# Optimization experiments

Hardware: AMD Instinct MI355X
Metric: run time of the kernel (lower is better)

Reference implementation:

```python
import jax, jax.numpy as jnp
import numpy as np

# Frankenstein DNC dims (from __init__ defaults, L reduced 16->8 for memory budget)
X = 47764; H = 128; L = 8; VT = 3620; W = 32; R = 8; N = 512; BS = 1
D = X + R * W + 2 * H            # RNN_Unit input width = 48276
ET = W * R + 3 * W + 5 * R + 3   # interface width = 395
EPS = 1e-8


def setup_inputs() -> dict:
    key = jax.random.key(0)
    ks = jax.random.split(key, 16)
    su = 1.0 / np.sqrt(H)          # nn.Linear default-style scale
    sv = 1.0 / np.sqrt(VT)
    se = 1.0 / np.sqrt(ET)
    u = lambda k, shp, s: jax.random.uniform(k, shp, jnp.float32, -s, s)
    return {
        'x_in': jax.random.normal(ks[0], (BS, X), jnp.float32),
        # stacked per-layer LSTM-gate weights (L, D, H) / biases (L, H)
        'W_i': u(ks[1], (L, D, H), su), 'b_i': u(ks[2], (L, H), su),
        'W_f': u(ks[3], (L, D, H), su), 'b_f': u(ks[4], (L, H), su),
        'W_o': u(ks[5], (L, D, H), su), 'b_o': u(ks[6], (L, H), su),
        'W_s': u(ks[7], (L, D, H), su), 'b_s': u(ks[8], (L, H), su),
        'W_y': u(ks[9], (L * H, VT), sv),
        'W_E': u(ks[10], (L * H, ET), se),
        'W_r': u(ks[11], (W * R, VT), sv),
        # memory / state buffers (requires_grad=False in torch)
        'memory': jax.random.uniform(ks[12], (N, W), jnp.float32, -1.0, 1.0),
        'last_read_vector': jnp.zeros((BS, W, R), jnp.float32),
        'hidden_prev': jnp.zeros((BS, L, H), jnp.float32),
        'old_states': jnp.zeros((L, BS, H), jnp.float32),
        'precedence': jnp.zeros((BS, N), jnp.float32),
        'linkage': jnp.zeros((BS, N, N), jnp.float32),
        'last_read_weightings': jnp.zeros((BS, N, R), jnp.float32),
        'last_usage': jnp.zeros((BS, N), jnp.float32),
        'last_write_weighting': jnp.zeros((BS, N), jnp.float32),
    }


def reference(x_in, W_i, b_i, W_f, b_f, W_o, b_o, W_s, b_s, W_y, W_E, W_r,
              memory, last_read_vector, hidden_prev, old_states, precedence,
              linkage, last_read_weightings, last_usage, last_write_weighting):
    # ---- controller: L stacked LSTM-like units, sequential over layers ----
    input_x_t = jnp.concatenate([x_in, last_read_vector.reshape(BS, -1)], axis=1)
    hpt = jnp.transpose(hidden_prev, (1, 0, 2))  # (L, BS, H)

    def layer(h_prev_layer, xs):
        Wi, bi, Wf, bf, Wo, bo, Ws, bs_, hp, os_ = xs
        si = jnp.concatenate([input_x_t, hp, h_prev_layer], axis=1)  # (BS, D)
        ig = jax.nn.sigmoid(si @ Wi + bi)
        fg = jax.nn.sigmoid(si @ Wf + bf)
        st = fg * os_ + ig * jnp.tanh(si @ Ws + bs_)
        og = jax.nn.sigmoid(si @ Wo + bo)
        h = og * jnp.tanh(st)
        return h, h

    _, hs = jax.lax.scan(layer, jnp.zeros((BS, H), x_in.dtype),
                         (W_i, b_i, W_f, b_f, W_o, b_o, W_s, b_s, hpt, old_states))
    flat = jnp.transpose(hs, (1, 0, 2)).reshape(BS, L * H)
    output = flat @ W_y
    E = flat @ W_E

    # ---- interface vector parsing ----
    i0 = 0
    read_keys = E[:, :W * R].reshape(BS, W, R); i0 = W * R
    read_strengths = 1.0 - jax.nn.log_sigmoid(E[:, i0:i0 + R]); i0 += R
    write_key = E[:, i0:i0 + W]; i0 += W
    write_strength = 1.0 - jax.nn.log_sigmoid(E[:, i0:i0 + 1]); i0 += 1
    erase = jax.nn.sigmoid(E[:, i0:i0 + W]); i0 += W
    write_vec = E[:, i0:i0 + W]; i0 += W
    free_gates = jax.nn.sigmoid(E[:, i0:i0 + R]); i0 += R
    alloc_gate = jax.nn.sigmoid(E[:, i0:i0 + 1]); i0 += 1
    write_gate = jax.nn.sigmoid(E[:, i0:i0 + 1]); i0 += 1
    read_modes = jax.nn.softmax(E[:, i0:i0 + 3 * R].reshape(BS, R, 3), axis=2)

    # ---- memory retention, usage, allocation ----
    psi = jnp.prod(1.0 - free_gates[:, None, :] * last_read_weightings, axis=2)  # (BS,N)
    usage = (last_usage + last_write_weighting - last_usage * last_write_weighting) * psi
    idx = jnp.argsort(usage, axis=1)
    su = jnp.take_along_axis(usage, idx, axis=1)
    cp = jnp.cumprod(su, axis=1)
    excl = jnp.concatenate([jnp.ones((BS, 1), usage.dtype), cp[:, :-1]], axis=1)
    alloc = jnp.take_along_axis((1.0 - su) * excl, jnp.argsort(idx, axis=1), axis=1)

    # ---- write weighting (content + allocation) ----
    Mn = memory / jnp.maximum(jnp.linalg.norm(memory, axis=1, keepdims=True), EPS)
    kn = write_key / jnp.maximum(jnp.linalg.norm(write_key, axis=1, keepdims=True), EPS)
    cw = jax.nn.softmax(write_strength * (kn @ Mn.T), axis=1)  # (BS,N)
    ww = write_gate * (alloc_gate * alloc + (1.0 - alloc_gate) * cw)

    # ---- write to memory (bs == 1) ----
    memory_new = memory * (1.0 - jnp.einsum('bn,bw->nw', ww, erase)) \
                 + jnp.einsum('bn,bw->nw', ww, write_vec)

    # ---- temporal linkage ----
    Lm = (1.0 - ww[:, :, None] - ww[:, None, :]) * linkage \
         + ww[:, :, None] * precedence[:, None, :]
    Lm = Lm * (1.0 - jnp.eye(N, dtype=Lm.dtype))[None]
    fw = jnp.einsum('bij,bjr->bir', Lm, last_read_weightings)   # forward weighting
    bw = jnp.einsum('bji,bjr->bir', Lm, last_read_weightings)   # backward weighting

    # ---- read weightings and read vectors ----
    Mn2 = memory_new / jnp.maximum(jnp.linalg.norm(memory_new, axis=1, keepdims=True), EPS)
    knr = read_keys / jnp.maximum(jnp.linalg.norm(read_keys, axis=1, keepdims=True), EPS)
    cr = jax.nn.softmax(read_strengths[:, None, :] * jnp.einsum('nw,bwr->bnr', Mn2, knr), axis=1)
    rw = bw * read_modes[:, None, :, 0] + cr * read_modes[:, None, :, 1] \
         + fw * read_modes[:, None, :, 2]                        # (BS,N,R)
    rv = jnp.einsum('nw,bnr->bwr', memory_new, rw)               # (BS,W,R)

    y = output + rv.reshape(BS, W * R) @ W_r                     # (BS, v_t)
    return y
```

## Files before the change

### kernel.cpp

```cpp
#include <hip/hip_runtime.h>
#include <math.h>

#define XDIM 47764
#define HDIM 128
#define LDIM 8
#define VTDIM 3620
#define WDIM 32
#define RDIM 8
#define NDIM 512
#define RW 256
#define DDIM 48276
#define FIXED 48148
#define ETDIM 395
#define EPSV 1e-8f

#define CHUNK 768
#define NCHUNK 63
#define K1_COMPUTE (32 * NCHUNK)
#define K1_COPYB 128

#define OFF_FIXED   258048
#define OFF_WREC    262144
#define OFF_FLAT    786432
#define OFF_ERAW    787456
#define OFF_WW      787968
#define OFF_MEMNEW  788480
#define OFF_CR      804864
#define OFF_RM      808960
#define OFF_FW      808992
#define OFF_BW      813088
#define OFF_RV      817184

typedef float f4 __attribute__((ext_vector_type(4)));

__device__ __forceinline__ f4 ntload4(const float* p) {
    return __builtin_nontemporal_load((const f4*)p);
}

__device__ inline float sigm(float x) { return 1.f / (1.f + expf(-x)); }
__device__ inline float log_sigmoid(float x) {
    return (x >= 0.f) ? -log1pf(expf(-x)) : (x - log1pf(expf(x)));
}

__global__ __launch_bounds__(256) void k1_partial(
    const float* __restrict__ x_in, const float* __restrict__ lrv,
    const float* __restrict__ hprev,
    const float* __restrict__ Wi, const float* __restrict__ Wf,
    const float* __restrict__ Wo, const float* __restrict__ Ws,
    float* __restrict__ ws, float* __restrict__ out)
{
    const int bid = blockIdx.x;
    const int t   = threadIdx.x;

    if (bid >= K1_COMPUTE) {
        int cb = bid - K1_COMPUTE;
        #pragma unroll
        for (int r = 0; r < 4; ++r) {
            int idx4  = cb * 1024 + r * 256 + t;
            int flat  = idx4 << 2;
            int combo = flat >> 14;
            int rem   = flat & 16383;
            int j = rem >> 7, h = rem & 127;
            int g = combo >> 3, l = combo & 7;
            const float* Wg = (g == 0) ? Wi : (g == 1) ? Wf : (g == 2) ? Wo : Ws;
            float4 v = *reinterpret_cast<const float4*>(
                Wg + ((size_t)l * DDIM + FIXED + j) * HDIM + h);
            *reinterpret_cast<float4*>(ws + OFF_WREC + flat) = v;
        }
        if (cb == 0) { ws[OFF_ERAW + t] = 0.f; ws[OFF_ERAW + 256 + t] = 0.f; }
        else if (cb == 1) {
            #pragma unroll
            for (int r = 0; r < 8; ++r) out[r * 256 + t] = 0.f;
        } else if (cb == 2) {
            #pragma unroll
            for (int r = 0; r < 7; ++r) {
                int v = 2048 + r * 256 + t;
                if (v < VTDIM) out[v] = 0.f;
            }
        }
        return;
    }

    const int combo = bid / NCHUNK;
    const int chunk = bid % NCHUNK;
    const int g = combo >> 3, l = combo & 7;
    const float* __restrict__ Wg = (g == 0) ? Wi : (g == 1) ? Wf : (g == 2) ? Wo : Ws;
    const int d0 = chunk * CHUNK;

    __shared__ float s_lds[CHUNK];
    for (int i = t; i < CHUNK; i += 256) {
        int d = d0 + i;
        float v = 0.f;
        if (d < XDIM)            v = x_in[d];
        else if (d < XDIM + RW)  v = lrv[d - XDIM];
        else if (d < FIXED)      v = hprev[l * HDIM + (d - XDIM - RW)];
        s_lds[i] = v;
    }
    __syncthreads();

    const int c4 = t & 15;
    const int p  = t >> 4;
    const int r0 = p * 48;
    const float* wp = Wg + ((size_t)l * DDIM + d0 + r0) * HDIM + (c4 << 2);

    f4 a = {0.f, 0.f, 0.f, 0.f};
    f4 b = {0.f, 0.f, 0.f, 0.f};

    if (chunk != NCHUNK - 1) {
        #pragma unroll 4
        for (int i = 0; i < 48; ++i) {
            float s = s_lds[r0 + i];
            const f4 w0 = ntload4(wp);
            const f4 w1 = ntload4(wp + 64);
            wp += HDIM;
            a += s * w0;
            b += s * w1;
        }
    } else {
        for (int i = 0; i < 48; ++i) {
            if (d0 + r0 + i >= FIXED) break;
            float s = s_lds[r0 + i];
            const f4 w0 = ntload4(wp);
            const f4 w1 = ntload4(wp + 64);
            wp += HDIM;
            a += s * w0;
            b += s * w1;
        }
    }

    __shared__ f4 red[16][32];
    red[p][c4]      = a;
    red[p][c4 + 16] = b;
    __syncthreads();
    if (t < 32) {
        f4 s = red[0][t];
        #pragma unroll
        for (int q = 1; q < 16; ++q) s += red[q][t];
        float* fx = ws + OFF_FIXED + combo * HDIM + (t << 2);
        atomicAdd(fx + 0, s.x);
        atomicAdd(fx + 1, s.y);
        atomicAdd(fx + 2, s.z);
        atomicAdd(fx + 3, s.w);
    }
}

__global__ __launch_bounds__(1024) void k3_recurrent(
    const float* __restrict__ bi, const float* __restrict__ bf,
    const float* __restrict__ bo, const float* __restrict__ bs,
    const float* __restrict__ old_states, float* __restrict__ ws)
{
    const int t = threadIdx.x;
    const int g = t >> 8;
    const int q = (t >> 7) & 1;
    const int h = t & 127;

    __shared__ float hp[128];
    __shared__ float gl[4][2][128];

    float fx[8];
    const float* bg = (g == 0) ? bi : (g == 1) ? bf : (g == 2) ? bo : bs;
    if (q == 0) {
        #pragma unroll
        for (int l = 0; l < LDIM; ++l)
            fx[l] = ws[OFF_FIXED + (g * 8 + l) * HDIM + h] + bg[l * HDIM + h];
    }
    if (t < 128) hp[t] = 0.f;
    __syncthreads();

    for (int l = 0; l < LDIM; ++l) {
        int combo = g * 8 + l;
        float acc = (q == 0) ? fx[l] : 0.f;
        const float* wr = ws + OFF_WREC + (size_t)combo * 16384 + (q << 6) * 128 + h;
        #pragma unroll 8
        for (int j = 0; j < 64; ++j) acc += hp[(q << 6) + j] * wr[j * 128];
        gl[g][q][h] = acc;
        __syncthreads();
        if (t < 128) {
            float ig = sigm(gl[0][0][t] + gl[0][1][t]);
            float fg = sigm(gl[1][0][t] + gl[1][1][t]);
            float og = sigm(gl[2][0][t] + gl[2][1][t]);
            float ss = tanhf(gl[3][0][t] + gl[3][1][t]);
            float st = fg * old_states[l * HDIM + t] + ig * ss;
            float hn = og * tanhf(st);
            hp[t] = hn;
            ws[OFF_FLAT + l * HDIM + t] = hn;
        }
        __syncthreads();
    }
}

__global__ __launch_bounds__(256) void k45_out_E(
    const float* __restrict__ Wy, const float* __restrict__ We,
    float* __restrict__ dout, float* __restrict__ ws)
{
    const int blk = blockIdx.x, t = threadIdx.x;
    if (blk < 240) {
        int vt = blk % 15, kc = blk / 15;
        __shared__ float fl[64];
        if (t < 64) fl[t] = ws[OFF_FLAT + kc * 64 + t];
        __syncthreads();
        int v = vt * 256 + t;
        if (v < VTDIM) {
            float acc = 0.f;
            const float* Wp = Wy + (size_t)kc * 64 * VTDIM + v;
            #pragma unroll 8
            for (int k = 0; k < 64; ++k) acc += fl[k] * Wp[(size_t)k * VTDIM];
            atomicAdd(&dout[v], acc);
        }
    } else {
        int kc = blk - 240;
        __shared__ float fl2[128];
        if (t < 128) fl2[t] = ws[OFF_FLAT + kc * 128 + t];
        __syncthreads();
        if (t < ETDIM) {
            float acc = 0.f;
            const float* Wp = We + (size_t)kc * 128 * ETDIM + t;
            #pragma unroll 8
            for (int k = 0; k < 128; ++k) acc += fl2[k] * Wp[k * ETDIM];
            atomicAdd(&ws[OFF_ERAW + t], acc);
        }
    }
}

__global__ __launch_bounds__(512) void k6_small(
    const float* __restrict__ memory, const float* __restrict__ lrw,
    const float* __restrict__ lu, const float* __restrict__ lww,
    float* __restrict__ ws)
{
    const int t = threadIdx.x;
    const int lane = t & 63, wid = t >> 6;
    __shared__ float Es[400];
    __shared__ float rk[256], wk[32], er[32], wv[32], fgs[8], rs_s[8], rm[24], scal[3];
    __shared__ float u_s[512];
    __shared__ float wred[8];
    __shared__ float wred8[8][8];
    __shared__ float srk[8];

    if (t < ETDIM) Es[t] = ws[OFF_ERAW + t];
    __syncthreads();

    if (t < 256)                 rk[t] = Es[t];
    if (t >= 256 && t < 264)     rs_s[t - 256] = 1.f - log_sigmoid(Es[t]);
    if (t >= 264 && t < 296)     wk[t - 264] = Es[t];
    if (t == 296)                scal[0] = 1.f - log_sigmoid(Es[296]);
    if (t >= 297 && t < 329)     er[t - 297] = sigm(Es[t]);
    if (t >= 329 && t < 361)     wv[t - 329] = Es[t];
    if (t >= 361 && t < 369)     fgs[t - 361] = sigm(Es[t]);
    if (t == 369)                scal[1] = sigm(Es[369]);
    if (t == 370)                scal[2] = sigm(Es[370]);
    if (t >= 384 && t < 392) {
        int r = t - 384;
        float a = Es[371 + 3*r], b = Es[372 + 3*r], c = Es[373 + 3*r];
        float mx = fmaxf(a, fmaxf(b, c));
        float ea = expf(a - mx), eb = expf(b - mx), ec = expf(c - mx);
        float s = ea + eb + ec;
        rm[3*r] = ea / s; rm[3*r + 1] = eb / s; rm[3*r + 2] = ec / s;
    }
    __syncthreads();

    float psi = 1.f;
    #pragma unroll
    for (int r = 0; r < 8; ++r) psi *= 1.f - fgs[r] * lrw[t * 8 + r];
    float ua = lu[t], ub = lww[t];
    float u_t = (ua + ub - ua * ub) * psi;
    u_s[t] = u_t;
    __syncthreads();

    float prod = 1.f;
    for (int j = 0; j < 512; ++j) {
        float uj = u_s[j];
        bool before = (uj < u_t) || (uj == u_t && j < t);
        prod *= before ? uj : 1.f;
    }
    float alloc_t = (1.f - u_t) * prod;

    float s2 = 0.f;
    #pragma unroll
    for (int w = 0; w < 32; ++w) s2 += wk[w] * wk[w];
    float wkinv = 1.f / fmaxf(sqrtf(s2), EPSV);

    float mrow[32];
    float dotv = 0.f, nn = 0.f;
    #pragma unroll
    for (int w = 0; w < 32; ++w) {
        float m = memory[t * 32 + w];
        mrow[w] = m; dotv += m * wk[w]; nn += m * m;
    }
    float score = scal[0] * wkinv * dotv / fmaxf(sqrtf(nn), EPSV);
    float v = score;
    #pragma unroll
    for (int o = 32; o > 0; o >>= 1) v = fmaxf(v, __shfl_xor(v, o));
    if (lane == 0) wred[wid] = v;
    __syncthreads();
    float mx = wred[0];
    #pragma unroll
    for (int qq = 1; qq < 8; ++qq) mx = fmaxf(mx, wred[qq]);
    __syncthreads();
    float e = expf(score - mx);
    v = e;
    #pragma unroll
    for (int o = 32; o > 0; o >>= 1) v += __shfl_xor(v, o);
    if (lane == 0) wred[wid] = v;
    __syncthreads();
    float ssum = 0.f;
    #pragma unroll
    for (int qq = 0; qq < 8; ++qq) ssum += wred[qq];
    float cwv = e / ssum;

    float wwn = scal[2] * (scal[1] * alloc_t + (1.f - scal[1]) * cwv);
    ws[OFF_WW + t] = wwn;

    float nn2 = 0.f;
    #pragma unroll
    for (int w = 0; w < 32; ++w) {
        float mn = mrow[w] * (1.f - wwn * er[w]) + wwn * wv[w];
        mrow[w] = mn; nn2 += mn * mn;
        ws[OFF_MEMNEW + t * 32 + w] = mn;
    }
    float inv2 = 1.f / fmaxf(sqrtf(nn2), EPSV);

    if (t < 8) {
        float s3 = 0.f;
        #pragma unroll
        for (int w = 0; w < 32; ++w) { float x = rk[w * 8 + t]; s3 += x * x; }
        srk[t] = rs_s[t] / fmaxf(sqrtf(s3), EPSV);
    }
    __syncthreads();

    float sc[8];
    #pragma unroll
    for (int r = 0; r < 8; ++r) {
        float d2 = 0.f;
        #pragma unroll
        for (int w = 0; w < 32; ++w) d2 += mrow[w] * rk[w * 8 + r];
        sc[r] = srk[r] * inv2 * d2;
    }
    #pragma unroll
    for (int r = 0; r < 8; ++r) {
        float x = sc[r];
        #pragma unroll
        for (int o = 32; o > 0; o >>= 1) x = fmaxf(x, __shfl_xor(x, o));
        if (lane == 0) wred8[wid][r] = x;
    }
    __syncthreads();
    float mxr[8];
    #pragma unroll
    for (int r = 0; r < 8; ++r) {
        float m = wred8[0][r];
        #pragma unroll
        for (int qq = 1; qq < 8; ++qq) m = fmaxf(m, wred8[qq][r]);
        mxr[r] = m;
    }
    __syncthreads();
    float ex[8];
    #pragma unroll
    for (int r = 0; r < 8; ++r) {
        ex[r] = expf(sc[r] - mxr[r]);
        float x = ex[r];
        #pragma unroll
        for (int o = 32; o > 0; o >>= 1) x += __shfl_xor(x, o);
        if (lane == 0) wred8[wid][r] = x;
    }
    __syncthreads();
    #pragma unroll
    for (int r = 0; r < 8; ++r) {
        float sm = 0.f;
        #pragma unroll
        for (int qq = 0; qq < 8; ++qq) sm += wred8[qq][r];
        ws[OFF_CR + t * 8 + r] = ex[r] / sm;
    }
    if (t < 24) ws[OFF_RM + t] = rm[t];
}

__global__ __launch_bounds__(256) void k7_linkage(
    const float* __restrict__ linkage, const float* __restrict__ prec,
    const float* __restrict__ lrw, float* __restrict__ ws)
{
    __shared__ float lrw_s[4096];
    __shared__ float ww_s[512];
    __shared__ float red2[2048];
    const int t = threadIdx.x, blk = blockIdx.x;
    for (int i = t; i < 4096; i += 256) lrw_s[i] = lrw[i];
    for (int i = t; i < 512; i += 256)  ww_s[i] = ws[OFF_WW + i];
    __syncthreads();

    if (blk < 512) {
        const int i = blk;
        const float ww_i = ww_s[i];
        float facc[8] = {0,0,0,0,0,0,0,0};
        for (int j = t; j < 512; j += 256) {
            float Lm = (j == i) ? 0.f
                     : (1.f - ww_i - ww_s[j]) * linkage[(size_t)i * 512 + j] + ww_i * prec[j];
            #pragma unroll
            for (int r = 0; r < 8; ++r) facc[r] += Lm * lrw_s[j * 8 + r];
        }
        #pragma unroll
        for (int r = 0; r < 8; ++r) red2[t * 8 + r] = facc[r];
        __syncthreads();
        for (int s = 128; s > 0; s >>= 1) {
            if (t < s) {
                #pragma unroll
                for (int r = 0; r < 8; ++r) red2[t * 8 + r] += red2[(t + s) * 8 + r];
            }
            __syncthreads();
        }
        if (t < 8) ws[OFF_FW + i * 8 + t] = red2[t];
    } else {
        const int bb = blk - 512;
        const int ii = t & 63, p = t >> 6;
        const int i = bb * 64 + ii;
        const float ww_i = ww_s[i], prec_i = prec[i];
        float bacc[8] = {0,0,0,0,0,0,0,0};
        for (int j = p * 128; j < p * 128 + 128; ++j) {
            float lj  = linkage[(size_t)j * 512 + i];
            float wwj = ww_s[j];
            float Lm  = (j == i) ? 0.f : (1.f - wwj - ww_i) * lj + wwj * prec_i;
            #pragma unroll
            for (int r = 0; r < 8; ++r) bacc[r] += Lm * lrw_s[j * 8 + r];
        }
        #pragma unroll
        for (int r = 0; r < 8; ++r) red2[t * 8 + r] = bacc[r];
        __syncthreads();
        if (p == 0) {
            #pragma unroll
            for (int r = 0; r < 8; ++r) {
                float s = red2[t * 8 + r] + red2[(t + 64) * 8 + r]
                        + red2[(t + 128) * 8 + r] + red2[(t + 192) * 8 + r];
                ws[OFF_BW + i * 8 + r] = s;
            }
        }
    }
}

__global__ __launch_bounds__(256) void k8a_rv(float* __restrict__ ws)
{
    __shared__ float mn_s[NDIM * 32];
    __shared__ float rw_s[NDIM * 8];
    __shared__ float rred[8][32][8];
    __shared__ float rm_s[24];
    const int t = threadIdx.x;

    for (int i = t; i < NDIM * 8; i += 256)
        *reinterpret_cast<float4*>(mn_s + (i << 2)) =
            *reinterpret_cast<const float4*>(ws + OFF_MEMNEW + (i << 2));
    if (t < 24) rm_s[t] = ws[OFF_RM + t];
    __syncthreads();

    for (int idx = t; idx < 4096; idx += 256) {
        int r = idx & 7;
        rw_s[idx] = ws[OFF_BW + idx] * rm_s[r * 3]
                  + ws[OFF_CR + idx] * rm_s[r * 3 + 1]
                  + ws[OFF_FW + idx] * rm_s[r * 3 + 2];
    }
    __syncthreads();

    const int g = t >> 5, w = t & 31;
    float acc[8] = {0,0,0,0,0,0,0,0};
    for (int n = g * 64; n < g * 64 + 64; ++n) {
        float m = mn_s[n * 32 + w];
        #pragma unroll
        for (int r = 0; r < 8; ++r) acc[r] += m * rw_s[n * 8 + r];
    }
    #pragma unroll
    for (int r = 0; r < 8; ++r) rred[g][w][r] = acc[r];
    __syncthreads();
    {
        int w2 = t >> 3, r2 = t & 7;
        float s = 0.f;
        #pragma unroll
        for (int qq = 0; qq < 8; ++qq) s += rred[qq][w2][r2];
        ws[OFF_RV + w2 * 8 + r2] = s;
    }
}

__global__ __launch_bounds__(256) void k8b_wr(
    const float* __restrict__ Wr, float* __restrict__ dout,
    const float* __restrict__ ws)
{
    const int blk = blockIdx.x, t = threadIdx.x;
    const int vt = blk % 15, kc = blk / 15;
    __shared__ float rv_s[64];
    if (t < 64) rv_s[t] = ws[OFF_RV + kc * 64 + t];
    __syncthreads();
    int v = vt * 256 + t;
    if (v < VTDIM) {
        float acc = 0.f;
        const float* Wp = Wr + (size_t)kc * 64 * VTDIM + v;
        #pragma unroll 8
        for (int k = 0; k < 64; ++k) acc += rv_s[k] * Wp[(size_t)k * VTDIM];
        atomicAdd(&dout[v], acc);
    }
}

extern "C" void kernel_launch(void* const* d_in, const int* in_sizes, int n_in,
                              void* d_out, int out_size, void* d_ws, size_t ws_size,
                              hipStream_t stream)
{
    const float* x_in   = (const float*)d_in[0];
    const float* Wi     = (const float*)d_in[1];
    const float* bi     = (const float*)d_in[2];
    const float* Wf     = (const float*)d_in[3];
    const float* bf     = (const float*)d_in[4];
    const float* Wo     = (const float*)d_in[5];
    const float* bo     = (const float*)d_in[6];
    const float* Wss    = (const float*)d_in[7];
    const float* bs     = (const float*)d_in[8];
    const float* Wy     = (const float*)d_in[9];
    const float* We     = (const float*)d_in[10];
    const float* Wr     = (const float*)d_in[11];
    const float* memory = (const float*)d_in[12];
    const float* lrv    = (const float*)d_in[13];
    const float* hprev  = (const float*)d_in[14];
    const float* old_st = (const float*)d_in[15];
    const float* prec   = (const float*)d_in[16];
    const float* linkage= (const float*)d_in[17];
    const float* lrw    = (const float*)d_in[18];
    const float* lu     = (const float*)d_in[19];
    const float* lww    = (const float*)d_in[20];
    float* out = (float*)d_out;
    float* ws  = (float*)d_ws;

    hipMemsetAsync((void*)(ws + OFF_FIXED), 0, 32 * HDIM * sizeof(float), stream);

    k1_partial<<<K1_COMPUTE + K1_COPYB, 256, 0, stream>>>(
        x_in, lrv, hprev, Wi, Wf, Wo, Wss, ws, out);
    k3_recurrent<<<1, 1024, 0, stream>>>(bi, bf, bo, bs, old_st, ws);
    k45_out_E<<<248, 256, 0, stream>>>(Wy, We, out, ws);
    k6_small<<<1, 512, 0, stream>>>(memory, lrw, lu, lww, ws);
    k7_linkage<<<520, 256, 0, stream>>>(linkage, prec, lrw, ws);
    k8a_rv<<<1, 256, 0, stream>>>(ws);
    k8b_wr<<<60, 256, 0, stream>>>(Wr, out, ws);
}
```

Measured before the change: 267.8 us.

## Fuse tail kernels into one cooperative grid-synced kernel and drop atomics

Replaces the six post-GEMV kernels with a single cooperative kernel of 256 blocks that separates its stages with grid.sync, removing launch gaps between small serial stages. The k1 atomics into the fixed-gate accumulator are replaced by per-chunk partial writes that the fused kernel reduces, and the memset is removed. The output and erase-vector GEMVs now write their results directly, so the zeroing stores in k1 go away. Several single-block stages still leave most of the grid idle, and each grid.sync has its own cost.

Result: slower. 383.9 us (+43.4%).

```diff
diff --git a/kernel.cpp b/kernel.cpp
--- a/kernel.cpp
+++ b/kernel.cpp
@@ -1,5 +1,8 @@
 #include <hip/hip_runtime.h>
+#include <hip/hip_cooperative_groups.h>
 #include <math.h>
+
+namespace cg = cooperative_groups;
 
 #define XDIM 47764
 #define HDIM 128
@@ -19,6 +22,7 @@
 #define K1_COMPUTE (32 * NCHUNK)
 #define K1_COPYB 128
 
+#define OFF_PARTIAL 0
 #define OFF_FIXED   258048
 #define OFF_WREC    262144
 #define OFF_FLAT    786432
@@ -47,7 +51,7 @@
     const float* __restrict__ hprev,
     const float* __restrict__ Wi, const float* __restrict__ Wf,
     const float* __restrict__ Wo, const float* __restrict__ Ws,
-    float* __restrict__ ws, float* __restrict__ out)
+    float* __restrict__ ws)
 {
     const int bid = blockIdx.x;
     const int t   = threadIdx.x;
@@ -67,17 +71,6 @@
                 Wg + ((size_t)l * DDIM + FIXED + j) * HDIM + h);
             *reinterpret_cast<float4*>(ws + OFF_WREC + flat) = v;
         }
-        if (cb == 0) { ws[OFF_ERAW + t] = 0.f; ws[OFF_ERAW + 256 + t] = 0.f; }
-        else if (cb == 1) {
-            #pragma unroll
-            for (int r = 0; r < 8; ++r) out[r * 256 + t] = 0.f;
-        } else if (cb == 2) {
-            #pragma unroll
-            for (int r = 0; r < 7; ++r) {
-                int v = 2048 + r * 256 + t;
-                if (v < VTDIM) out[v] = 0.f;
-            }
-        }
         return;
     }
 
@@ -136,359 +129,386 @@
         f4 s = red[0][t];
         #pragma unroll
         for (int q = 1; q < 16; ++q) s += red[q][t];
-        float* fx = ws + OFF_FIXED + combo * HDIM + (t << 2);
-        atomicAdd(fx + 0, s.x);
-        atomicAdd(fx + 1, s.y);
-        atomicAdd(fx + 2, s.z);
-        atomicAdd(fx + 3, s.w);
+        *reinterpret_cast<f4*>(ws + OFF_PARTIAL +
+            ((size_t)(combo * NCHUNK + chunk)) * HDIM + (t << 2)) = s;
     }
 }
 
-__global__ __launch_bounds__(1024) void k3_recurrent(
+__global__ __launch_bounds__(512) void tail_fused(
     const float* __restrict__ bi, const float* __restrict__ bf,
     const float* __restrict__ bo, const float* __restrict__ bs,
-    const float* __restrict__ old_states, float* __restrict__ ws)
-{
-    const int t = threadIdx.x;
-    const int g = t >> 8;
-    const int q = (t >> 7) & 1;
-    const int h = t & 127;
-
-    __shared__ float hp[128];
-    __shared__ float gl[4][2][128];
-
-    float fx[8];
-    const float* bg = (g == 0) ? bi : (g == 1) ? bf : (g == 2) ? bo : bs;
-    if (q == 0) {
-        #pragma unroll
-        for (int l = 0; l < LDIM; ++l)
-            fx[l] = ws[OFF_FIXED + (g * 8 + l) * HDIM + h] + bg[l * HDIM + h];
-    }
-    if (t < 128) hp[t] = 0.f;
-    __syncthreads();
-
-    for (int l = 0; l < LDIM; ++l) {
-        int combo = g * 8 + l;
-        float acc = (q == 0) ? fx[l] : 0.f;
-        const float* wr = ws + OFF_WREC + (size_t)combo * 16384 + (q << 6) * 128 + h;
-        #pragma unroll 8
-        for (int j = 0; j < 64; ++j) acc += hp[(q << 6) + j] * wr[j * 128];
-        gl[g][q][h] = acc;
-        __syncthreads();
-        if (t < 128) {
-            float ig = sigm(gl[0][0][t] + gl[0][1][t]);
-            float fg = sigm(gl[1][0][t] + gl[1][1][t]);
-            float og = sigm(gl[2][0][t] + gl[2][1][t]);
-            float ss = tanhf(gl[3][0][t] + gl[3][1][t]);
-            float st = fg * old_states[l * HDIM + t] + ig * ss;
-            float hn = og * tanhf(st);
-            hp[t] = hn;
-            ws[OFF_FLAT + l * HDIM + t] = hn;
-        }
-        __syncthreads();
-    }
-}
-
-__global__ __launch_bounds__(256) void k45_out_E(
+    const float* __restrict__ old_st,
     const float* __restrict__ Wy, const float* __restrict__ We,
-    float* __restrict__ dout, float* __restrict__ ws)
-{
-    const int blk = blockIdx.x, t = threadIdx.x;
-    if (blk < 240) {
-        int vt = blk % 15, kc = blk / 15;
-        __shared__ float fl[64];
-        if (t < 64) fl[t] = ws[OFF_FLAT + kc * 64 + t];
-        __syncthreads();
-        int v = vt * 256 + t;
-        if (v < VTDIM) {
-            float acc = 0.f;
-            const float* Wp = Wy + (size_t)kc * 64 * VTDIM + v;
-            #pragma unroll 8
-            for (int k = 0; k < 64; ++k) acc += fl[k] * Wp[(size_t)k * VTDIM];
-            atomicAdd(&dout[v], acc);
-        }
-    } else {
-        int kc = blk - 240;
-        __shared__ float fl2[128];
-        if (t < 128) fl2[t] = ws[OFF_FLAT + kc * 128 + t];
-        __syncthreads();
-        if (t < ETDIM) {
-            float acc = 0.f;
-            const float* Wp = We + (size_t)kc * 128 * ETDIM + t;
-            #pragma unroll 8
-            for (int k = 0; k < 128; ++k) acc += fl2[k] * Wp[k * ETDIM];
-            atomicAdd(&ws[OFF_ERAW + t], acc);
-        }
-    }
-}
-
-__global__ __launch_bounds__(512) void k6_small(
+    const float* __restrict__ Wr,
     const float* __restrict__ memory, const float* __restrict__ lrw,
     const float* __restrict__ lu, const float* __restrict__ lww,
-    float* __restrict__ ws)
+    const float* __restrict__ linkage, const float* __restrict__ prec,
+    float* __restrict__ ws, float* __restrict__ out)
 {
-    const int t = threadIdx.x;
+    cg::grid_group grid = cg::this_grid();
+    const int blk = blockIdx.x, t = threadIdx.x;
     const int lane = t & 63, wid = t >> 6;
-    __shared__ float Es[400];
-    __shared__ float rk[256], wk[32], er[32], wv[32], fgs[8], rs_s[8], rm[24], scal[3];
-    __shared__ float u_s[512];
-    __shared__ float wred[8];
-    __shared__ float wred8[8][8];
-    __shared__ float srk[8];
-
-    if (t < ETDIM) Es[t] = ws[OFF_ERAW + t];
-    __syncthreads();
-
-    if (t < 256)                 rk[t] = Es[t];
-    if (t >= 256 && t < 264)     rs_s[t - 256] = 1.f - log_sigmoid(Es[t]);
-    if (t >= 264 && t < 296)     wk[t - 264] = Es[t];
-    if (t == 296)                scal[0] = 1.f - log_sigmoid(Es[296]);
-    if (t >= 297 && t < 329)     er[t - 297] = sigm(Es[t]);
-    if (t >= 329 && t < 361)     wv[t - 329] = Es[t];
-    if (t >= 361 && t < 369)     fgs[t - 361] = sigm(Es[t]);
-    if (t == 369)                scal[1] = sigm(Es[369]);
-    if (t == 370)                scal[2] = sigm(Es[370]);
-    if (t >= 384 && t < 392) {
-        int r = t - 384;
-        float a = Es[371 + 3*r], b = Es[372 + 3*r], c = Es[373 + 3*r];
-        float mx = fmaxf(a, fmaxf(b, c));
-        float ea = expf(a - mx), eb = expf(b - mx), ec = expf(c - mx);
-        float s = ea + eb + ec;
-        rm[3*r] = ea / s; rm[3*r + 1] = eb / s; rm[3*r + 2] = ec / s;
-    }
-    __syncthreads();
-
-    float psi = 1.f;
-    #pragma unroll
-    for (int r = 0; r < 8; ++r) psi *= 1.f - fgs[r] * lrw[t * 8 + r];
-    float ua = lu[t], ub = lww[t];
-    float u_t = (ua + ub - ua * ub) * psi;
-    u_s[t] = u_t;
-    __syncthreads();
-
-    float prod = 1.f;
-    for (int j = 0; j < 512; ++j) {
-        float uj = u_s[j];
-        bool before = (uj < u_t) || (uj == u_t && j < t);
-        prod *= before ? uj : 1.f;
-    }
-    float alloc_t = (1.f - u_t) * prod;
-
-    float s2 = 0.f;
-    #pragma unroll
-    for (int w = 0; w < 32; ++w) s2 += wk[w] * wk[w];
-    float wkinv = 1.f / fmaxf(sqrtf(s2), EPSV);
-
-    float mrow[32];
-    float dotv = 0.f, nn = 0.f;
-    #pragma unroll
-    for (int w = 0; w < 32; ++w) {
-        float m = memory[t * 32 + w];
-        mrow[w] = m; dotv += m * wk[w]; nn += m * m;
-    }
-    float score = scal[0] * wkinv * dotv / fmaxf(sqrtf(nn), EPSV);
-    float v = score;
-    #pragma unroll
-    for (int o = 32; o > 0; o >>= 1) v = fmaxf(v, __shfl_xor(v, o));
-    if (lane == 0) wred[wid] = v;
-    __syncthreads();
-    float mx = wred[0];
-    #pragma unroll
-    for (int qq = 1; qq < 8; ++qq) mx = fmaxf(mx, wred[qq]);
-    __syncthreads();
-    float e = expf(score - mx);
-    v = e;
-    #pragma unroll
-    for (int o = 32; o > 0; o >>= 1) v += __shfl_xor(v, o);
-    if (lane == 0) wred[wid] = v;
-    __syncthreads();
-    float ssum = 0.f;
-    #pragma unroll
-    for (int qq = 0; qq < 8; ++qq) ssum += wred[qq];
-    float cwv = e / ssum;
-
-    float wwn = scal[2] * (scal[1] * alloc_t + (1.f - scal[1]) * cwv);
-    ws[OFF_WW + t] = wwn;
-
-    float nn2 = 0.f;
-    #pragma unroll
-    for (int w = 0; w < 32; ++w) {
-        float mn = mrow[w] * (1.f - wwn * er[w]) + wwn * wv[w];
-        mrow[w] = mn; nn2 += mn * mn;
-        ws[OFF_MEMNEW + t * 32 + w] = mn;
-    }
-    float inv2 = 1.f / fmaxf(sqrtf(nn2), EPSV);
-
-    if (t < 8) {
-        float s3 = 0.f;
-        #pragma unroll
-        for (int w = 0; w < 32; ++w) { float x = rk[w * 8 + t]; s3 += x * x; }
-        srk[t] = rs_s[t] / fmaxf(sqrtf(s3), EPSV);
-    }
-    __syncthreads();
-
-    float sc[8];
-    #pragma unroll
-    for (int r = 0; r < 8; ++r) {
-        float d2 = 0.f;
-        #pragma unroll
-        for (int w = 0; w < 32; ++w) d2 += mrow[w] * rk[w * 8 + r];
-        sc[r] = srk[r] * inv2 * d2;
-    }
-    #pragma unroll
-    for (int r = 0; r < 8; ++r) {
-        float x = sc[r];
-        #pragma unroll
-        for (int o = 32; o > 0; o >>= 1) x = fmaxf(x, __shfl_xor(x, o));
-        if (lane == 0) wred8[wid][r] = x;
-    }
-    __syncthreads();
-    float mxr[8];
-    #pragma unroll
-    for (int r = 0; r < 8; ++r) {
-        float m = wred8[0][r];
-        #pragma unroll
-        for (int qq = 1; qq < 8; ++qq) m = fmaxf(m, wred8[qq][r]);
-        mxr[r] = m;
-    }
-    __syncthreads();
-    float ex[8];
-    #pragma unroll
-    for (int r = 0; r < 8; ++r) {
-        ex[r] = expf(sc[r] - mxr[r]);
-        float x = ex[r];
-        #pragma unroll
-        for (int o = 32; o > 0; o >>= 1) x += __shfl_xor(x, o);
-        if (lane == 0) wred8[wid][r] = x;
-    }
-    __syncthreads();
-    #pragma unroll
-    for (int r = 0; r < 8; ++r) {
-        float sm = 0.f;
-        #pragma unroll
-        for (int qq = 0; qq < 8; ++qq) sm += wred8[qq][r];
-        ws[OFF_CR + t * 8 + r] = ex[r] / sm;
-    }
-    if (t < 24) ws[OFF_RM + t] = rm[t];
-}
-
-__global__ __launch_bounds__(256) void k7_linkage(
-    const float* __restrict__ linkage, const float* __restrict__ prec,
-    const float* __restrict__ lrw, float* __restrict__ ws)
-{
-    __shared__ float lrw_s[4096];
-    __shared__ float ww_s[512];
-    __shared__ float red2[2048];
-    const int t = threadIdx.x, blk = blockIdx.x;
-    for (int i = t; i < 4096; i += 256) lrw_s[i] = lrw[i];
-    for (int i = t; i < 512; i += 256)  ww_s[i] = ws[OFF_WW + i];
-    __syncthreads();
-
-    if (blk < 512) {
-        const int i = blk;
-        const float ww_i = ww_s[i];
-        float facc[8] = {0,0,0,0,0,0,0,0};
-        for (int j = t; j < 512; j += 256) {
-            float Lm = (j == i) ? 0.f
-                     : (1.f - ww_i - ww_s[j]) * linkage[(size_t)i * 512 + j] + ww_i * prec[j];
-            #pragma unroll
-            for (int r = 0; r < 8; ++r) facc[r] += Lm * lrw_s[j * 8 + r];
-        }
-        #pragma unroll
-        for (int r = 0; r < 8; ++r) red2[t * 8 + r] = facc[r];
-        __syncthreads();
-        for (int s = 128; s > 0; s >>= 1) {
-            if (t < s) {
-                #pragma unroll
-                for (int r = 0; r < 8; ++r) red2[t * 8 + r] += red2[(t + s) * 8 + r];
+
+    __shared__ float smem[6272];
+
+    if (blk < 32) {
+        const int seg = t >> 7, h = t & 127;
+        float acc = 0.f;
+        for (int c = seg; c < NCHUNK; c += 4)
+            acc += ws[OFF_PARTIAL + (size_t)(blk * NCHUNK + c) * HDIM + h];
+        smem[seg * 128 + h] = acc;
+        __syncthreads();
+        if (t < 128) {
+            int g = blk >> 3, l = blk & 7;
+            const float* bg = (g == 0) ? bi : (g == 1) ? bf : (g == 2) ? bo : bs;
+            ws[OFF_FIXED + blk * HDIM + t] =
+                smem[t] + smem[128 + t] + smem[256 + t] + smem[384 + t]
+                + bg[l * HDIM + t];
+        }
+    }
+    grid.sync();
+
+    if (blk == 0) {
+        float* hp = smem;
+        float* gl = smem + 128;
+        const int g = t >> 7, h = t & 127;
+        float fx[LDIM];
+        #pragma unroll
+        for (int l = 0; l < LDIM; ++l)
+            fx[l] = ws[OFF_FIXED + (g * 8 + l) * HDIM + h];
+        if (t < 128) hp[t] = 0.f;
+        __syncthreads();
+        for (int l = 0; l < LDIM; ++l) {
+            const float* wr = ws + OFF_WREC + (size_t)(g * 8 + l) * 16384 + h;
+            float acc = fx[l];
+            #pragma unroll 16
+            for (int j = 0; j < 128; ++j) acc += hp[j] * wr[j * 128];
+            gl[g * 128 + h] = acc;
+            __syncthreads();
+            if (t < 128) {
+                float ig = sigm(gl[t]);
+                float fg = sigm(gl[128 + t]);
+                float og = sigm(gl[256 + t]);
+                float ss = tanhf(gl[384 + t]);
+                float st = fg * old_st[l * HDIM + t] + ig * ss;
+                float hn = og * tanhf(st);
+                hp[t] = hn;
+                ws[OFF_FLAT + l * HDIM + t] = hn;
             }
             __syncthreads();
         }
-        if (t < 8) ws[OFF_FW + i * 8 + t] = red2[t];
-    } else {
-        const int bb = blk - 512;
-        const int ii = t & 63, p = t >> 6;
-        const int i = bb * 64 + ii;
-        const float ww_i = ww_s[i], prec_i = prec[i];
-        float bacc[8] = {0,0,0,0,0,0,0,0};
-        for (int j = p * 128; j < p * 128 + 128; ++j) {
-            float lj  = linkage[(size_t)j * 512 + i];
-            float wwj = ww_s[j];
-            float Lm  = (j == i) ? 0.f : (1.f - wwj - ww_i) * lj + wwj * prec_i;
-            #pragma unroll
-            for (int r = 0; r < 8; ++r) bacc[r] += Lm * lrw_s[j * 8 + r];
-        }
-        #pragma unroll
-        for (int r = 0; r < 8; ++r) red2[t * 8 + r] = bacc[r];
-        __syncthreads();
-        if (p == 0) {
+    }
+    grid.sync();
+
+    if (blk < 227) {
+        float* flat_s = smem;
+        float* pr     = smem + 1024;
+        flat_s[t]       = ws[OFF_FLAT + t];
+        flat_s[512 + t] = ws[OFF_FLAT + 512 + t];
+        __syncthreads();
+        const int ks = t >> 4, v16 = t & 15;
+        const int v = blk * 16 + v16;
+        float acc = 0.f;
+        if (v < VTDIM) {
+            const float* Wp = Wy + (size_t)(ks * 32) * VTDIM + v;
+            #pragma unroll 8
+            for (int k = 0; k < 32; ++k)
+                acc += flat_s[ks * 32 + k] * Wp[(size_t)k * VTDIM];
+        }
+        pr[ks * 16 + v16] = acc;
+        __syncthreads();
+        if (t < 16) {
+            float s = 0.f;
+            #pragma unroll
+            for (int q = 0; q < 32; ++q) s += pr[q * 16 + t];
+            int vv = blk * 16 + t;
+            if (vv < VTDIM) out[vv] = s;
+        }
+    } else if (blk < 235) {
+        float* flat_s = smem;
+        float* pr     = smem + 1024;
+        flat_s[t]       = ws[OFF_FLAT + t];
+        flat_s[512 + t] = ws[OFF_FLAT + 512 + t];
+        __syncthreads();
+        const int ks = t >> 6, e64 = t & 63;
+        const int e = (blk - 227) * 64 + e64;
+        float acc = 0.f;
+        if (e < ETDIM) {
+            const float* Wp = We + (size_t)(ks * 128) * ETDIM + e;
+            #pragma unroll 8
+            for (int k = 0; k < 128; ++k)
+                acc += flat_s[ks * 128 + k] * Wp[(size_t)k * ETDIM];
+        }
+        pr[ks * 64 + e64] = acc;
+        __syncthreads();
+        if (t < 64) {
+            float s = 0.f;
+            #pragma unroll
+            for (int q = 0; q < 8; ++q) s += pr[q * 64 + t];
+            int ee = (blk - 227) * 64 + t;
+            if (ee < ETDIM) ws[OFF_ERAW + ee] = s;
+        }
+    }
+    grid.sync();
+
+    if (blk == 0) {
+        float* Es   = smem;
+        float* rk   = smem + 416;
+        float* wk   = smem + 672;
+        float* er   = smem + 704;
+        float* wvv  = smem + 736;
+        float* fgs  = smem + 768;
+        float* rss  = smem + 776;
+        float* rm   = smem + 784;
+        float* scal = smem + 808;
+        float* u_s  = smem + 816;
+        float* wred = smem + 1328;
+        float* wred8= smem + 1336;
+        float* srk  = smem + 1400;
+
+        if (t < ETDIM) Es[t] = ws[OFF_ERAW + t];
+        __syncthreads();
+
+        if (t < 256)                 rk[t] = Es[t];
+        if (t >= 256 && t < 264)     rss[t - 256] = 1.f - log_sigmoid(Es[t]);
+        if (t >= 264 && t < 296)     wk[t - 264] = Es[t];
+        if (t == 296)                scal[0] = 1.f - log_sigmoid(Es[296]);
+        if (t >= 297 && t < 329)     er[t - 297] = sigm(Es[t]);
+        if (t >= 329 && t < 361)     wvv[t - 329] = Es[t];
+        if (t >= 361 && t < 369)     fgs[t - 361] = sigm(Es[t]);
+        if (t == 369)                scal[1] = sigm(Es[369]);
+        if (t == 370)                scal[2] = sigm(Es[370]);
+        if (t >= 384 && t < 392) {
+            int r = t - 384;
+            float a = Es[371 + 3*r], b = Es[372 + 3*r], c = Es[373 + 3*r];
+            float mx = fmaxf(a, fmaxf(b, c));
+            float ea = expf(a - mx), eb = expf(b - mx), ec = expf(c - mx);
+            float s = ea + eb + ec;
+            rm[3*r] = ea / s; rm[3*r + 1] = eb / s; rm[3*r + 2] = ec / s;
+        }
+        __syncthreads();
+
+        float psi = 1.f;
+        #pragma unroll
+        for (int r = 0; r < 8; ++r) psi *= 1.f - fgs[r] * lrw[t * 8 + r];
+        float ua = lu[t], ub = lww[t];
+        float u_t = (ua + ub - ua * ub) * psi;
+        u_s[t] = u_t;
+        __syncthreads();
+
+        float prod = 1.f;
+        for (int j = 0; j < 512; ++j) {
+            float uj = u_s[j];
+            bool before = (uj < u_t) || (uj == u_t && j < t);
+            prod *= before ? uj : 1.f;
+        }
+        float alloc_t = (1.f - u_t) * prod;
+
+        float s2 = 0.f;
+        #pragma unroll
+        for (int w = 0; w < 32; ++w) s2 += wk[w] * wk[w];
+        float wkinv = 1.f / fmaxf(sqrtf(s2), EPSV);
+
+        float mrow[32];
+        float dotv = 0.f, nn = 0.f;
+        #pragma unroll
+        for (int w = 0; w < 32; ++w) {
+            float m = memory[t * 32 + w];
+            mrow[w] = m; dotv += m * wk[w]; nn += m * m;
+        }
+        float score = scal[0] * wkinv * dotv / fmaxf(sqrtf(nn), EPSV);
+        float v = score;
+        #pragma unroll
+        for (int o = 32; o > 0; o >>= 1) v = fmaxf(v, __shfl_xor(v, o));
+        if (lane == 0) wred[wid] = v;
+        __syncthreads();
+        float mx = wred[0];
+        #pragma unroll
+        for (int qq = 1; qq < 8; ++qq) mx = fmaxf(mx, wred[qq]);
+        __syncthreads();
+        float e = expf(score - mx);
+        v = e;
+        #pragma unroll
+        for (int o = 32; o > 0; o >>= 1) v += __shfl_xor(v, o);
+        if (lane == 0) wred[wid] = v;
+        __syncthreads();
+        float ssum = 0.f;
+        #pragma unroll
+        for (int qq = 0; qq < 8; ++qq) ssum += wred[qq];
+        float cwv = e / ssum;
+
+        float wwn = scal[2] * (scal[1] * alloc_t + (1.f - scal[1]) * cwv);
+        ws[OFF_WW + t] = wwn;
+
+        float nn2 = 0.f;
+        #pragma unroll
+        for (int w = 0; w < 32; ++w) {
+            float mn = mrow[w] * (1.f - wwn * er[w]) + wwn * wvv[w];
+            mrow[w] = mn; nn2 += mn * mn;
+            ws[OFF_MEMNEW + t * 32 + w] = mn;
+        }
+        float inv2 = 1.f / fmaxf(sqrtf(nn2), EPSV);
+
+        if (t < 8) {
+            float s3 = 0.f;
+            #pragma unroll
+            for (int w = 0; w < 32; ++w) { float x = rk[w * 8 + t]; s3 += x * x; }
+            srk[t] = rss[t] / fmaxf(sqrtf(s3), EPSV);
+        }
+        __syncthreads();
+
+        float sc[8];
+        #pragma unroll
+        for (int r = 0; r < 8; ++r) {
+            float d2 = 0.f;
+            #pragma unroll
+            for (int w = 0; w < 32; ++w) d2 += mrow[w] * rk[w * 8 + r];
+            sc[r] = srk[r] * inv2 * d2;
+        }
+        #pragma unroll
+        for (int r = 0; r < 8; ++r) {
+            float x = sc[r];
+            #pragma unroll
+            for (int o = 32; o > 0; o >>= 1) x = fmaxf(x, __shfl_xor(x, o));
+            if (lane == 0) wred8[wid * 8 + r] = x;
+        }
+        __syncthreads();
+        float mxr[8];
+        #pragma unroll
+        for (int r = 0; r < 8; ++r) {
+            float m = wred8[r];
+            #pragma unroll
+            for (int qq = 1; qq < 8; ++qq) m = fmaxf(m, wred8[qq * 8 + r]);
+            mxr[r] = m;
+        }
+        __syncthreads();
+        float ex[8];
+        #pragma unroll
+        for (int r = 0; r < 8; ++r) {
+            ex[r] = expf(sc[r] - mxr[r]);
+            float x = ex[r];
+            #pragma unroll
+            for (int o = 32; o > 0; o >>= 1) x += __shfl_xor(x, o);
+            if (lane == 0) wred8[wid * 8 + r] = x;
+        }
+        __syncthreads();
+        #pragma unroll
+        for (int r = 0; r < 8; ++r) {
+            float sm = 0.f;
+            #pragma unroll
+            for (int qq = 0; qq < 8; ++qq) sm += wred8[qq * 8 + r];
+            ws[OFF_CR + t * 8 + r] = ex[r] / sm;
+        }
+        if (t < 24) ws[OFF_RM + t] = rm[t];
+    }
+    grid.sync();
+
+    {
+        float* lrw_s  = smem;
+        float* ww_s   = smem + 4608;
+        float* rowred = smem + 5120;
+        for (int i = t; i < 4096; i += 512)
+            lrw_s[(i >> 3) * 9 + (i & 7)] = lrw[i];
+        ww_s[t] = ws[OFF_WW + t];
+        __syncthreads();
+
+        const float pt = prec[t];
+        const float wwt = ww_s[t];
+        float la[8];
+        #pragma unroll
+        for (int r = 0; r < 8; ++r) la[r] = lrw_s[t * 9 + r];
+
+        #pragma unroll
+        for (int pass = 0; pass < 4; ++pass) {
+            const int i = blk * 2 + (pass & 1);
+            float lm;
+            if (pass < 2) {
+                float lj = linkage[(size_t)i * 512 + t];
+                lm = (t == i) ? 0.f : (1.f - ww_s[i] - wwt) * lj + ww_s[i] * pt;
+            } else {
+                float lj = linkage[(size_t)t * 512 + i];
+                lm = (t == i) ? 0.f : (1.f - wwt - ww_s[i]) * lj + wwt * prec[i];
+            }
             #pragma unroll
             for (int r = 0; r < 8; ++r) {
-                float s = red2[t * 8 + r] + red2[(t + 64) * 8 + r]
-                        + red2[(t + 128) * 8 + r] + red2[(t + 192) * 8 + r];
-                ws[OFF_BW + i * 8 + r] = s;
+                float v = lm * la[r];
+                #pragma unroll
+                for (int o = 32; o > 0; o >>= 1) v += __shfl_xor(v, o);
+                if (lane == 0) rowred[wid * 8 + r] = v;
             }
-        }
-    }
-}
-
-__global__ __launch_bounds__(256) void k8a_rv(float* __restrict__ ws)
-{
-    __shared__ float mn_s[NDIM * 32];
-    __shared__ float rw_s[NDIM * 8];
-    __shared__ float rred[8][32][8];
-    __shared__ float rm_s[24];
-    const int t = threadIdx.x;
-
-    for (int i = t; i < NDIM * 8; i += 256)
-        *reinterpret_cast<float4*>(mn_s + (i << 2)) =
-            *reinterpret_cast<const float4*>(ws + OFF_MEMNEW + (i << 2));
-    if (t < 24) rm_s[t] = ws[OFF_RM + t];
-    __syncthreads();
-
-    for (int idx = t; idx < 4096; idx += 256) {
-        int r = idx & 7;
-        rw_s[idx] = ws[OFF_BW + idx] * rm_s[r * 3]
-                  + ws[OFF_CR + idx] * rm_s[r * 3 + 1]
-                  + ws[OFF_FW + idx] * rm_s[r * 3 + 2];
-    }
-    __syncthreads();
-
-    const int g = t >> 5, w = t & 31;
-    float acc[8] = {0,0,0,0,0,0,0,0};
-    for (int n = g * 64; n < g * 64 + 64; ++n) {
-        float m = mn_s[n * 32 + w];
-        #pragma unroll
-        for (int r = 0; r < 8; ++r) acc[r] += m * rw_s[n * 8 + r];
-    }
-    #pragma unroll
-    for (int r = 0; r < 8; ++r) rred[g][w][r] = acc[r];
-    __syncthreads();
-    {
-        int w2 = t >> 3, r2 = t & 7;
-        float s = 0.f;
-        #pragma unroll
-        for (int qq = 0; qq < 8; ++qq) s += rred[qq][w2][r2];
-        ws[OFF_RV + w2 * 8 + r2] = s;
-    }
-}
-
-__global__ __launch_bounds__(256) void k8b_wr(
-    const float* __restrict__ Wr, float* __restrict__ dout,
-    const float* __restrict__ ws)
-{
-    const int blk = blockIdx.x, t = threadIdx.x;
-    const int vt = blk % 15, kc = blk / 15;
-    __shared__ float rv_s[64];
-    if (t < 64) rv_s[t] = ws[OFF_RV + kc * 64 + t];
-    __syncthreads();
-    int v = vt * 256 + t;
-    if (v < VTDIM) {
+            __syncthreads();
+            if (t < 8) {
+                float s = 0.f;
+                #pragma unroll
+                for (int w = 0; w < 8; ++w) s += rowred[w * 8 + t];
+                ws[((pass < 2) ? OFF_FW : OFF_BW) + i * 8 + t] = s;
+            }
+            __syncthreads();
+        }
+    }
+    grid.sync();
+
+    if (blk == 0) {
+        float* rw_s = smem;
+        float* rred = smem + 4096;
+        float* rm_s = smem + 6144;
+        if (t < 24) rm_s[t] = ws[OFF_RM + t];
+        __syncthreads();
+        for (int idx = t; idx < 4096; idx += 512) {
+            int r = idx & 7;
+            rw_s[idx] = ws[OFF_BW + idx] * rm_s[r * 3]
+                      + ws[OFF_CR + idx] * rm_s[r * 3 + 1]
+                      + ws[OFF_FW + idx] * rm_s[r * 3 + 2];
+        }
+        __syncthreads();
+
+        const int g = t >> 5, w = t & 31;
+        float acc[8] = {0,0,0,0,0,0,0,0};
+        for (int n = g * 32; n < g * 32 + 32; ++n) {
+            float m = ws[OFF_MEMNEW + n * 32 + w];
+            #pragma unroll
+            for (int r = 0; r < 8; ++r) acc[r] += m * rw_s[n * 8 + r];
+        }
+        #pragma unroll
+        for (int r = 0; r < 8; ++r) {
+            float v = acc[r] + __shfl_xor(acc[r], 32);
+            if (lane < 32) rred[(wid * 32 + w) * 8 + r] = v;
+        }
+        __syncthreads();
+        if (t < 256) {
+            int w2 = t >> 3, r2 = t & 7;
+            float s = 0.f;
+            #pragma unroll
+            for (int qq = 0; qq < 8; ++qq) s += rred[(qq * 32 + w2) * 8 + r2];
+            ws[OFF_RV + w2 * 8 + r2] = s;
+        }
+    }
+    grid.sync();
+
+    if (blk < 114) {
+        float* rv_s = smem;
+        float* pr   = smem + 256;
+        if (t < 256) rv_s[t] = ws[OFF_RV + t];
+        __syncthreads();
+        const int ks = t >> 5, v32 = t & 31;
+        const int v = blk * 32 + v32;
         float acc = 0.f;
-        const float* Wp = Wr + (size_t)kc * 64 * VTDIM + v;
-        #pragma unroll 8
-        for (int k = 0; k < 64; ++k) acc += rv_s[k] * Wp[(size_t)k * VTDIM];
-        atomicAdd(&dout[v], acc);
+        if (v < VTDIM) {
+            const float* Wp = Wr + (size_t)(ks * 16) * VTDIM + v;
+            #pragma unroll
+            for (int k = 0; k < 16; ++k) acc += rv_s[ks * 16 + k] * Wp[(size_t)k * VTDIM];
+        }
+        pr[ks * 32 + v32] = acc;
+        __syncthreads();
+        if (t < 32) {
+            int vv = blk * 32 + t;
+            if (vv < VTDIM) {
+                float s = 0.f;
+                #pragma unroll
+                for (int q = 0; q < 16; ++q) s += pr[q * 32 + t];
+                atomicAdd(&out[vv], s);
+            }
+        }
     }
 }
 
@@ -520,14 +540,15 @@
     float* out = (float*)d_out;
     float* ws  = (float*)d_ws;
 
-    hipMemsetAsync((void*)(ws + OFF_FIXED), 0, 32 * HDIM * sizeof(float), stream);
-
     k1_partial<<<K1_COMPUTE + K1_COPYB, 256, 0, stream>>>(
-        x_in, lrv, hprev, Wi, Wf, Wo, Wss, ws, out);
-    k3_recurrent<<<1, 1024, 0, stream>>>(bi, bf, bo, bs, old_st, ws);
-    k45_out_E<<<248, 256, 0, stream>>>(Wy, We, out, ws);
-    k6_small<<<1, 512, 0, stream>>>(memory, lrw, lu, lww, ws);
-    k7_linkage<<<520, 256, 0, stream>>>(linkage, prec, lrw, ws);
-    k8a_rv<<<1, 256, 0, stream>>>(ws);
-    k8b_wr<<<60, 256, 0, stream>>>(Wr, out, ws);
+        x_in, lrv, hprev, Wi, Wf, Wo, Wss, ws);
+
+    void* args[] = {
+        (void*)&bi, (void*)&bf, (void*)&bo, (void*)&bs, (void*)&old_st,
+        (void*)&Wy, (void*)&We, (void*)&Wr,
+        (void*)&memory, (void*)&lrw, (void*)&lu, (void*)&lww,
+        (void*)&linkage, (void*)&prec, (void*)&ws, (void*)&out
+    };
+    hipLaunchCooperativeKernel((void*)tail_fused, dim3(256), dim3(512),
+                               args, 0, stream);
 }
```
